# Performance work log

Hardware: AMD Instinct MI355X
Metric: run time of the kernel (lower is better)

## Reference

```python
import jax, jax.numpy as jnp
import numpy as np


def setup_inputs() -> dict:
    key = jax.random.key(0)
    ks = jax.random.split(key, 16)
    B, T, E, H, V = 64, 24, 512, 1024, 32000
    A = H  # attention_dim == hidden_size in original init
    s = 0.02  # init scale
    n = lambda k, shape: (jax.random.normal(k, shape, jnp.float32) * s)
    return {
        "features": jax.random.normal(ks[0], (B, E), jnp.float32),
        "captions": jax.random.randint(ks[1], (B, T), 0, V, dtype=jnp.int32),
        "lengths": jnp.full((B, 1), T + 1, dtype=jnp.int32),
        # learned parameters
        "emb": n(ks[2], (V, E)),
        "We": n(ks[3], (E, A)), "be": jnp.zeros((A,), jnp.float32),
        "Wd": n(ks[4], (H, A)), "bd": jnp.zeros((A,), jnp.float32),
        "va": n(ks[5], (A,)), "ba": jnp.zeros((), jnp.float32),
        "Wih": n(ks[6], (E, H)), "bih": jnp.zeros((H,), jnp.float32),
        "Wic": n(ks[7], (E, H)), "bic": jnp.zeros((H,), jnp.float32),
        "Wfb": n(ks[8], (H, E)), "bfb": jnp.zeros((E,), jnp.float32),
        "Wi": n(ks[9], (2 * E, 4 * H)), "Wh": n(ks[10], (H, 4 * H)),
        "bl": jnp.zeros((4 * H,), jnp.float32),
        "Wo": n(ks[11], (H, V)), "bo": jnp.zeros((V,), jnp.float32),
    }


def reference(features, captions, lengths, emb, We, be, Wd, bd, va, ba,
              Wih, bih, Wic, bic, Wfb, bfb, Wi, Wh, bl, Wo, bo):
    T = captions.shape[1]
    # embeddings = [features ; embed(captions)] -> [B, T+1, E]
    embeds = jnp.concatenate([features[:, None, :], emb[captions]], axis=1)
    mean_e = embeds.mean(axis=1)
    h = mean_e @ Wih + bih  # init_h
    c = mean_e @ Wic + bic  # init_c
    att1 = embeds @ We + be  # encoder projection, precomputed [B, L, A]

    def step(carry, emb_t):
        h, c = carry
        # additive attention over the full encoded sequence
        score = jnp.einsum('bla,a->bl', jax.nn.relu(att1 + (h @ Wd + bd)[:, None, :]), va) + ba
        alpha = jax.nn.softmax(score, axis=1)
        awe = jnp.einsum('bl,ble->be', alpha, embeds)
        gate = jax.nn.sigmoid(h @ Wfb + bfb)
        x = jnp.concatenate([emb_t, gate * awe], axis=-1)  # [B, 2E]
        z = x @ Wi + h @ Wh + bl
        i, f, g, o = jnp.split(z, 4, axis=-1)  # torch LSTM gate order i,f,g,o
        c = jax.nn.sigmoid(f) * c + jax.nn.sigmoid(i) * jnp.tanh(g)
        h = jax.nn.sigmoid(o) * jnp.tanh(c)
        return (h, c), h @ Wo + bo

    emb_seq = jnp.swapaxes(embeds[:, :T, :], 0, 1)  # [T, B, E]
    (_, _), logits = jax.lax.scan(step, (h, c), emb_seq)
    return jnp.swapaxes(logits, 0, 1)  # [B, T, V]
```

## Files before the change

### kernel.cpp

```cpp
#include <hip/hip_runtime.h>
#include <cstdio>
#include <cstdint>

#define B_ 64
#define T_ 24
#define L_ 25
#define E_ 512
#define H_ 1024
#define A_ 1024
#define V_ 32000
#define HCAT 5632

typedef unsigned short u16;
typedef short bf16x8 __attribute__((ext_vector_type(8)));
typedef float f32x4 __attribute__((ext_vector_type(4)));

__device__ __forceinline__ u16 f2bf(float f) {
    union { float f; unsigned int u; } v; v.f = f;
    unsigned int u = v.u;
    unsigned int r = (u + 0x7FFFu + ((u >> 16) & 1u)) >> 16;
    return (u16)r;
}
__device__ __forceinline__ float bf2f(u16 h) {
    union { unsigned int u; float f; } v; v.u = ((unsigned int)h) << 16;
    return v.f;
}
__device__ __forceinline__ void splitbf(float a, u16& hi, u16& lo) {
    hi = f2bf(a);
    lo = f2bf(a - bf2f(hi));
}
__device__ __forceinline__ float sigf(float x) { return 1.f / (1.f + __expf(-x)); }


__global__ void build_embeds(const float* __restrict__ features, const int* __restrict__ captions,
                             const float* __restrict__ emb, float* __restrict__ embeds,
                             float* __restrict__ mean_eT, u16* __restrict__ embsL2,
                             u16* __restrict__ embsA2) {
    int b = blockIdx.x; int e = threadIdx.x;
    float s = 0.f;
    for (int l = 0; l < L_; ++l) {
        float w;
        if (l == 0) w = features[b * E_ + e];
        else {
            int cap = captions[b * T_ + (l - 1)];
            w = emb[(size_t)cap * E_ + e];
        }
        embeds[(size_t)(b * L_ + l) * E_ + e] = w;
        s += w;
        u16 hi, lo; splitbf(w, hi, lo);
        size_t rl = (size_t)(b * L_ + l) * 1536;
        embsL2[rl + e] = hi; embsL2[rl + 512 + e] = lo; embsL2[rl + 1024 + e] = hi;
        if (l < T_) {
            size_t ra = (size_t)(l * 64 + b) * 1536;
            embsA2[ra + e] = hi; embsA2[ra + 512 + e] = lo; embsA2[ra + 1024 + e] = hi;
        }
    }
    mean_eT[e * B_ + b] = s * (1.f / 25.f);
}

__global__ void transpose_wo(const float* __restrict__ Wo, u16* __restrict__ WoT) {
    __shared__ float tile[32][33];
    int n0 = blockIdx.x * 32, k0 = blockIdx.y * 32;
    int tid = threadIdx.x;
    int tx = tid & 31, ty = tid >> 5;
    for (int i = ty; i < 32; i += 8)
        tile[i][tx] = Wo[(size_t)(k0 + i) * V_ + n0 + tx];
    __syncthreads();
    for (int i = ty; i < 32; i += 8)
        WoT[(size_t)(n0 + i) * H_ + k0 + tx] = f2bf(tile[tx][i]);
}

__global__ void tsplit(const float* __restrict__ W, u16* __restrict__ dst, int K, int srcld) {
    __shared__ float tile[32][33];
    int n0 = blockIdx.x * 32, k0 = blockIdx.y * 32;
    int tid = threadIdx.x;
    int tx = tid & 31, ty = tid >> 5;
    for (int i = ty; i < 32; i += 8)
        tile[i][tx] = W[(size_t)(k0 + i) * srcld + n0 + tx];
    __syncthreads();
    for (int i = ty; i < 32; i += 8) {
        float v = tile[tx][i];
        u16 hi, lo; splitbf(v, hi, lo);
        u16* d = dst + (size_t)(n0 + i) * (3 * K) + (k0 + tx);
        d[0] = hi; d[K] = hi; d[2 * K] = lo;
    }
}

__global__ __launch_bounds__(1024) void init_hc(const float* __restrict__ mean_eT,
                                                const float* __restrict__ Wih, const float* __restrict__ bih,
                                                const float* __restrict__ Wic, const float* __restrict__ bic,
                                                u16* __restrict__ h2, float* __restrict__ c) {
    int tid = threadIdx.x; int ny = tid & 15, r = tid >> 4;
    int col = blockIdx.x * 16 + ny;
    int cc = (col < H_) ? col : col - H_;
    const float* Wp = (col < H_) ? Wih : Wic;
    const float* bp = (col < H_) ? bih : bic;
    float acc = bp[cc];
    for (int k = 0; k < E_; ++k) acc += mean_eT[k * B_ + r] * Wp[(size_t)k * H_ + cc];
    if (col < H_) {
        u16 hi, lo; splitbf(acc, hi, lo);
        h2[(size_t)r * 3072 + cc] = hi;
        h2[(size_t)r * 3072 + 1024 + cc] = lo;
        h2[(size_t)r * 3072 + 2048 + cc] = hi;
    } else c[r * H_ + cc] = acc;
}

template<int BM, int BN>
__global__ __launch_bounds__(256) void gemm_split(const u16* __restrict__ A2, const u16* __restrict__ B2T,
                                                  const float* __restrict__ bias, float* __restrict__ C,
                                                  int K3, int ldc) {
    constexpr int LDS = 40;
    __shared__ u16 As[BM * LDS];
    __shared__ u16 Bs[BN * LDS];
    constexpr int FM = BM / 32, FN = BN / 32;
    constexpr int ACH = BM / 64, BCH = BN / 64;
    int m0 = blockIdx.x * BM, n0 = blockIdx.y * BN;
    int tid = threadIdx.x, lane = tid & 63, wid = tid >> 6;
    int wm = wid >> 1, wn = wid & 1;

    f32x4 acc[FM][FN];
#pragma unroll
    for (int m = 0; m < FM; ++m)
#pragma unroll
        for (int n = 0; n < FN; ++n) acc[m][n] = (f32x4){0.f, 0.f, 0.f, 0.f};

    const u16* agp[ACH]; u16* asw[ACH];
    const u16* bgp[BCH]; u16* bsw[BCH];
#pragma unroll
    for (int i = 0; i < ACH; ++i) {
        int id = i * 256 + tid; int row = id >> 2, q = id & 3;
        agp[i] = A2 + (size_t)(m0 + row) * K3 + q * 8;
        asw[i] = As + row * LDS + q * 8;
    }
#pragma unroll
    for (int i = 0; i < BCH; ++i) {
        int id = i * 256 + tid; int row = id >> 2, q = id & 3;
        bgp[i] = B2T + (size_t)(n0 + row) * K3 + q * 8;
        bsw[i] = Bs + row * LDS + q * 8;
    }
    int rsel = lane & 15, kg = (lane >> 4) * 8;
    const u16* ard[FM]; const u16* brd[FN];
#pragma unroll
    for (int m = 0; m < FM; ++m) ard[m] = As + (wm * (BM / 2) + m * 16 + rsel) * LDS + kg;
#pragma unroll
    for (int n = 0; n < FN; ++n) brd[n] = Bs + (wn * (BN / 2) + n * 16 + rsel) * LDS + kg;

    uint4 ar[ACH], br[BCH];
#pragma unroll
    for (int i = 0; i < ACH; ++i) ar[i] = *(const uint4*)(agp[i]);
#pragma unroll
    for (int i = 0; i < BCH; ++i) br[i] = *(const uint4*)(bgp[i]);

    int nk = K3 / 32;
    for (int k = 0; k < nk; ++k) {
#pragma unroll
        for (int i = 0; i < ACH; ++i) *(uint4*)(asw[i]) = ar[i];
#pragma unroll
        for (int i = 0; i < BCH; ++i) *(uint4*)(bsw[i]) = br[i];
        __syncthreads();
        if (k + 1 < nk) {
            int kt = (k + 1) * 32;
#pragma unroll
            for (int i = 0; i < ACH; ++i) ar[i] = *(const uint4*)(agp[i] + kt);
#pragma unroll
            for (int i = 0; i < BCH; ++i) br[i] = *(const uint4*)(bgp[i] + kt);
        }
        bf16x8 aF[FM], bF[FN];
#pragma unroll
        for (int m = 0; m < FM; ++m) aF[m] = *(const bf16x8*)(ard[m]);
#pragma unroll
        for (int n = 0; n < FN; ++n) bF[n] = *(const bf16x8*)(brd[n]);
#pragma unroll
        for (int m = 0; m < FM; ++m)
#pragma unroll
            for (int n = 0; n < FN; ++n)
                acc[m][n] = __builtin_amdgcn_mfma_f32_16x16x32_bf16(aF[m], bF[n], acc[m][n], 0, 0, 0);
        __syncthreads();
    }

    int r4 = (lane >> 4) * 4, cn = lane & 15;
#pragma unroll
    for (int n = 0; n < FN; ++n) {
        int gcol = n0 + wn * (BN / 2) + n * 16 + cn;
        float bv = bias[gcol];
#pragma unroll
        for (int m = 0; m < FM; ++m) {
            int gr = m0 + wm * (BM / 2) + m * 16 + r4;
#pragma unroll
            for (int reg = 0; reg < 4; ++reg)
                C[(size_t)(gr + reg) * ldc + gcol] = acc[m][n][reg] + bv;
        }
    }
}

template<int KITERS>
__global__ __launch_bounds__(256, 2) void gemm_sk(const u16* __restrict__ A2, const u16* __restrict__ B2T,
                                                  float* __restrict__ part, int K3, int N) {
    constexpr int BK = 128;
    constexpr int LDS = BK + 8;
    __shared__ u16 As[64 * LDS];
    __shared__ u16 Bs[64 * LDS];
    int n0 = blockIdx.x * 64;
    int ky = blockIdx.y;
    int k0 = ky * (BK * KITERS);
    int tid = threadIdx.x, lane = tid & 63, wid = tid >> 6;
    int wm = wid >> 1, wn = wid & 1;

    f32x4 acc[2][2];
#pragma unroll
    for (int m = 0; m < 2; ++m)
#pragma unroll
        for (int n = 0; n < 2; ++n) acc[m][n] = (f32x4){0.f, 0.f, 0.f, 0.f};

    int srow = tid >> 4, scq = tid & 15;
    const u16* agp[4]; u16* asw[4];
    const u16* bgp[4]; u16* bsw[4];
#pragma unroll
    for (int i = 0; i < 4; ++i) {
        int row = srow + i * 16;
        agp[i] = A2 + (size_t)row * K3 + k0 + scq * 8;
        asw[i] = As + row * LDS + scq * 8;
        bgp[i] = B2T + (size_t)(n0 + row) * K3 + k0 + scq * 8;
        bsw[i] = Bs + row * LDS + scq * 8;
    }
    int rsel = lane & 15, kg = (lane >> 4) * 8;
    const u16* ard[2]; const u16* brd[2];
#pragma unroll
    for (int m = 0; m < 2; ++m) ard[m] = As + (wm * 32 + m * 16 + rsel) * LDS + kg;
#pragma unroll
    for (int n = 0; n < 2; ++n) brd[n] = Bs + (wn * 32 + n * 16 + rsel) * LDS + kg;

    uint4 ar[4], br[4];
#pragma unroll
    for (int i = 0; i < 4; ++i) { ar[i] = *(const uint4*)(agp[i]); br[i] = *(const uint4*)(bgp[i]); }

    for (int it = 0; it < KITERS; ++it) {
#pragma unroll
        for (int i = 0; i < 4; ++i) { *(uint4*)(asw[i]) = ar[i]; *(uint4*)(bsw[i]) = br[i]; }
        __syncthreads();
        if (it + 1 < KITERS) {
            int kt = (it + 1) * BK;
#pragma unroll
            for (int i = 0; i < 4; ++i) {
                ar[i] = *(const uint4*)(agp[i] + kt);
                br[i] = *(const uint4*)(bgp[i] + kt);
            }
        }
#pragma unroll
        for (int kk = 0; kk < BK / 32; ++kk) {
            bf16x8 aF[2], bF[2];
#pragma unroll
            for (int m = 0; m < 2; ++m) aF[m] = *(const bf16x8*)(ard[m] + kk * 32);
#pragma unroll
            for (int n = 0; n < 2; ++n) bF[n] = *(const bf16x8*)(brd[n] + kk * 32);
#pragma unroll
            for (int m = 0; m < 2; ++m)
#pragma unroll
                for (int n = 0; n < 2; ++n)
                    acc[m][n] = __builtin_amdgcn_mfma_f32_16x16x32_bf16(aF[m], bF[n], acc[m][n], 0, 0, 0);
        }
        __syncthreads();
    }

    float* p = part + (size_t)ky * 64 * N;
    int r4 = (lane >> 4) * 4, cn = lane & 15;
#pragma unroll
    for (int n = 0; n < 2; ++n) {
        int gcol = n0 + wn * 32 + n * 16 + cn;
#pragma unroll
        for (int m = 0; m < 2; ++m) {
            int gr = wm * 32 + m * 16 + r4;
#pragma unroll
            for (int reg = 0; reg < 4; ++reg)
                p[(size_t)(gr + reg) * N + gcol] = acc[m][n][reg];
        }
    }
}


__global__ __launch_bounds__(256) void step_attn(const float* __restrict__ hpart, const float* __restrict__ att1,
                                                 const float* __restrict__ embeds, const float* __restrict__ va,
                                                 const float* __restrict__ bd, const float* __restrict__ bfb,
                                                 u16* __restrict__ x2s) {
    __shared__ float proj_s[1024], va_s[1024], sc_s[32], al_s[32];
    int b = blockIdx.x; int tid = threadIdx.x; int lane = tid & 63; int w = tid >> 6;
    for (int i = tid; i < 1024; i += 256) {
        float s = bd[i];
#pragma unroll
        for (int ky = 0; ky < 6; ++ky) s += hpart[(size_t)ky * 64 * HCAT + b * HCAT + i];
        proj_s[i] = s; va_s[i] = va[i];
    }
    __syncthreads();
    for (int l = w; l < L_; l += 4) {
        const float* arow = att1 + (size_t)(b * L_ + l) * A_;
        float p = 0.f;
        for (int a = lane; a < A_; a += 64) {
            float v = arow[a] + proj_s[a];
            p += fmaxf(v, 0.f) * va_s[a];
        }
        for (int off = 32; off; off >>= 1) p += __shfl_down(p, off);
        if (lane == 0) sc_s[l] = p;
    }
    __syncthreads();
    if (w == 0) {
        float s = (lane < L_) ? sc_s[lane] : -1e30f;
        float m = s;
        for (int off = 32; off; off >>= 1) m = fmaxf(m, __shfl_xor(m, off));
        float e = (lane < L_) ? __expf(s - m) : 0.f;
        float sum = e;
        for (int off = 32; off; off >>= 1) sum += __shfl_xor(sum, off);
        if (lane < L_) al_s[lane] = e / sum;
    }
    __syncthreads();
    for (int e = tid; e < E_; e += 256) {
        float aw = 0.f;
        for (int l = 0; l < L_; ++l) aw += al_s[l] * embeds[(size_t)(b * L_ + l) * E_ + e];
        float gp = bfb[e];
#pragma unroll
        for (int ky = 0; ky < 6; ++ky) gp += hpart[(size_t)ky * 64 * HCAT + b * HCAT + 1024 + e];
        float v = sigf(gp) * aw;
        u16 hi, lo; splitbf(v, hi, lo);
        x2s[(size_t)b * 1536 + e] = hi;
        x2s[(size_t)b * 1536 + 512 + e] = lo;
        x2s[(size_t)b * 1536 + 1024 + e] = hi;
    }
}

__global__ __launch_bounds__(256) void step_lstm(const float* __restrict__ zpart, const float* __restrict__ P1,
                                                 const float* __restrict__ hpart, float* __restrict__ c,
                                                 u16* __restrict__ h2, u16* __restrict__ hs_bf, int t) {
    int idx = blockIdx.x * 256 + threadIdx.x;
    int b = idx >> 10, n = idx & 1023;
    float zv[4];
#pragma unroll
    for (int g = 0; g < 4; ++g) {
        int col = g * 1024 + n;
        float s = P1[(size_t)(t * 64 + b) * 4096 + col];
#pragma unroll
        for (int ky = 0; ky < 3; ++ky) s += zpart[(size_t)ky * 64 * 4096 + b * 4096 + col];
#pragma unroll
        for (int ky = 0; ky < 6; ++ky) s += hpart[(size_t)ky * 64 * HCAT + b * HCAT + 1536 + col];
        zv[g] = s;
    }
    float cold = c[b * H_ + n];
    float cnew = sigf(zv[1]) * cold + sigf(zv[0]) * tanhf(zv[2]);
    float hh = sigf(zv[3]) * tanhf(cnew);
    c[b * H_ + n] = cnew;
    u16 hi, lo; splitbf(hh, hi, lo);
    h2[(size_t)b * 3072 + n] = hi;
    h2[(size_t)b * 3072 + 1024 + n] = lo;
    h2[(size_t)b * 3072 + 2048 + n] = hi;
    hs_bf[(size_t)(t * 64 + b) * 1024 + n] = f2bf(hh);
}

#define BMG 128
#define BNG 128
#define LDSS 40
#define NWG_M (T_ * B_ / BMG)
#define NWG_N (V_ / BNG)
#define NWG (NWG_M * NWG_N)

__global__ __launch_bounds__(256) void gemm_logits(const u16* __restrict__ Abf, const u16* __restrict__ Bbf,
                                                   const float* __restrict__ bo, float* __restrict__ out) {
    __shared__ u16 As[BMG * LDSS];
    __shared__ u16 Bs[BNG * LDSS];
    int lid = blockIdx.x;
    int wg = (lid & 7) * (NWG / 8) + (lid >> 3);
    int m0 = (wg % NWG_M) * BMG;
    int n0 = (wg / NWG_M) * BNG;
    int tid = threadIdx.x; int lane = tid & 63; int wid = tid >> 6;
    int wm = wid >> 1, wn = wid & 1;

    f32x4 acc[4][4];
#pragma unroll
    for (int m = 0; m < 4; ++m)
#pragma unroll
        for (int n = 0; n < 4; ++n) acc[m][n] = (f32x4){0.f, 0.f, 0.f, 0.f};

    int srow = tid >> 1;
    int shalf = tid & 1;
    const u16* ag = Abf + (size_t)(m0 + srow) * H_ + shalf * 16;
    const u16* bg = Bbf + (size_t)(n0 + srow) * H_ + shalf * 16;
    u16* asw = As + srow * LDSS + shalf * 16;
    u16* bsw = Bs + srow * LDSS + shalf * 16;

    int rsel = (lane & 15);
    int kg = (lane >> 4) * 8;

    uint4 a0 = *(const uint4*)(ag), a1 = *(const uint4*)(ag + 8);
    uint4 b0 = *(const uint4*)(bg), b1 = *(const uint4*)(bg + 8);

    for (int kt = 0; kt < H_; kt += 32) {
        *(uint4*)(asw) = a0; *(uint4*)(asw + 8) = a1;
        *(uint4*)(bsw) = b0; *(uint4*)(bsw + 8) = b1;
        __syncthreads();
        if (kt + 32 < H_) {
            a0 = *(const uint4*)(ag + kt + 32); a1 = *(const uint4*)(ag + kt + 40);
            b0 = *(const uint4*)(bg + kt + 32); b1 = *(const uint4*)(bg + kt + 40);
        }
        bf16x8 aF[4], bF[4];
#pragma unroll
        for (int m = 0; m < 4; ++m)
            aF[m] = *(const bf16x8*)(As + (wm * 64 + m * 16 + rsel) * LDSS + kg);
#pragma unroll
        for (int n = 0; n < 4; ++n)
            bF[n] = *(const bf16x8*)(Bs + (wn * 64 + n * 16 + rsel) * LDSS + kg);
#pragma unroll
        for (int m = 0; m < 4; ++m)
#pragma unroll
            for (int n = 0; n < 4; ++n)
                acc[m][n] = __builtin_amdgcn_mfma_f32_16x16x32_bf16(aF[m], bF[n], acc[m][n], 0, 0, 0);
        __syncthreads();
    }

    int r4 = (lane >> 4) * 4;
    int cn = lane & 15;
#pragma unroll
    for (int n = 0; n < 4; ++n) {
        int gn = n0 + wn * 64 + n * 16 + cn;
        float bv = bo[gn];
#pragma unroll
        for (int m = 0; m < 4; ++m) {
            int gmb = m0 + wm * 64 + m * 16 + r4;
#pragma unroll
            for (int reg = 0; reg < 4; ++reg) {
                int gm = gmb + reg;
                int b = gm & 63, t = gm >> 6;
                out[(size_t)(b * T_ + t) * V_ + gn] = acc[m][n][reg] + bv;
            }
        }
    }
}

extern "C" void kernel_launch(void* const* d_in, const int* in_sizes, int n_in,
                              void* d_out, int out_size, void* d_ws, size_t ws_size,
                              hipStream_t stream) {
    const float* features = (const float*)d_in[0];
    const int*   captions = (const int*)d_in[1];
    const float* emb = (const float*)d_in[3];
    const float* We  = (const float*)d_in[4];
    const float* be  = (const float*)d_in[5];
    const float* Wd  = (const float*)d_in[6];
    const float* bd  = (const float*)d_in[7];
    const float* va  = (const float*)d_in[8];
    const float* Wih = (const float*)d_in[10];
    const float* bih = (const float*)d_in[11];
    const float* Wic = (const float*)d_in[12];
    const float* bic = (const float*)d_in[13];
    const float* Wfb = (const float*)d_in[14];
    const float* bfb = (const float*)d_in[15];
    const float* Wi  = (const float*)d_in[16];
    const float* Wh  = (const float*)d_in[17];
    const float* bl  = (const float*)d_in[18];
    const float* Wo  = (const float*)d_in[19];
    const float* bo  = (const float*)d_in[20];
    float* out = (float*)d_out;

    char* ws = (char*)d_ws; size_t wo = 0;
    auto walloc = [&](size_t bytes) -> void* {
        void* p = ws + wo; wo += (bytes + 255) & ~(size_t)255; return p;
    };
    float* embeds  = (float*)walloc((size_t)B_ * L_ * E_ * 4);
    float* mean_eT = (float*)walloc((size_t)E_ * B_ * 4);
    u16*   embsL2  = (u16*)walloc((size_t)B_ * L_ * 1536 * 2);
    u16*   embsA2  = (u16*)walloc((size_t)T_ * B_ * 1536 * 2);
    u16*   h2      = (u16*)walloc((size_t)B_ * 3072 * 2);
    float* c       = (float*)walloc((size_t)B_ * H_ * 4);
    u16*   x2s     = (u16*)walloc((size_t)B_ * 1536 * 2);
    u16*   hs_bf   = (u16*)walloc((size_t)T_ * B_ * H_ * 2);
    u16*   WoT     = (u16*)walloc((size_t)V_ * H_ * 2);
    float* hpart   = (float*)walloc((size_t)6 * B_ * HCAT * 4);
    float* zpart   = (float*)walloc((size_t)3 * B_ * 4096 * 4);
    if (wo > ws_size) {
        fprintf(stderr, "kernel_launch: ws too small: need %zu have %zu\n", wo, ws_size);
        return;
    }

    char* ob = (char*)d_out; size_t oo = 0;
    auto oalloc = [&](size_t bytes) -> void* {
        void* p = ob + oo; oo += (bytes + 255) & ~(size_t)255; return p;
    };
    float* P1     = (float*)oalloc((size_t)T_ * B_ * 4096 * 4);
    u16*   WcatT2 = (u16*)oalloc((size_t)HCAT * 3072 * 2);
    u16*   WiT2a  = (u16*)oalloc((size_t)4096 * 1536 * 2);
    u16*   WiT2b  = (u16*)oalloc((size_t)4096 * 1536 * 2);
    u16*   WeT2   = (u16*)oalloc((size_t)1024 * 1536 * 2);
    float* att1   = (float*)oalloc((size_t)B_ * L_ * A_ * 4);

    build_embeds<<<B_, E_, 0, stream>>>(features, captions, emb, embeds, mean_eT, embsL2, embsA2);
    transpose_wo<<<dim3(V_ / 32, H_ / 32), 256, 0, stream>>>(Wo, WoT);
    tsplit<<<dim3(1024 / 32, 1024 / 32), 256, 0, stream>>>(Wd, WcatT2, 1024, 1024);
    tsplit<<<dim3(512 / 32, 1024 / 32), 256, 0, stream>>>(Wfb, WcatT2 + (size_t)1024 * 3072, 1024, 512);
    tsplit<<<dim3(4096 / 32, 1024 / 32), 256, 0, stream>>>(Wh, WcatT2 + (size_t)1536 * 3072, 1024, 4096);
    tsplit<<<dim3(4096 / 32, 512 / 32), 256, 0, stream>>>(Wi, WiT2a, 512, 4096);
    tsplit<<<dim3(4096 / 32, 512 / 32), 256, 0, stream>>>(Wi + (size_t)512 * 4096, WiT2b, 512, 4096);
    tsplit<<<dim3(1024 / 32, 512 / 32), 256, 0, stream>>>(We, WeT2, 512, 1024);
    init_hc<<<2 * H_ / 16, 1024, 0, stream>>>(mean_eT, Wih, bih, Wic, bic, h2, c);
    gemm_split<64, 64><<<dim3(1600 / 64, 1024 / 64), 256, 0, stream>>>(embsL2, WeT2, be, att1, 1536, 1024);
    gemm_split<128, 64><<<dim3(1536 / 128, 4096 / 64), 256, 0, stream>>>(embsA2, WiT2a, bl, P1, 1536, 4096);

    for (int t = 0; t < T_; ++t) {
        gemm_sk<4><<<dim3(HCAT / 64, 6), 256, 0, stream>>>(h2, WcatT2, hpart, 3072, HCAT);
        step_attn<<<B_, 256, 0, stream>>>(hpart, att1, embeds, va, bd, bfb, x2s);
        gemm_sk<4><<<dim3(4096 / 64, 3), 256, 0, stream>>>(x2s, WiT2b, zpart, 1536, 4096);
        step_lstm<<<B_ * H_ / 256, 256, 0, stream>>>(zpart, P1, hpart, c, h2, hs_bf, t);
    }

    gemm_logits<<<NWG, 256, 0, stream>>>(hs_bf, WoT, bo, out);
}
```

Before: 2.576 ms.

## Fuse recurrent loop into persistent kernel with grid barriers, merge weight prep kernels

```diff
diff --git a/kernel.cpp b/kernel.cpp
--- a/kernel.cpp
+++ b/kernel.cpp
@@ -58,23 +58,33 @@
     mean_eT[e * B_ + b] = s * (1.f / 25.f);
 }
 
-__global__ void transpose_wo(const float* __restrict__ Wo, u16* __restrict__ WoT) {
+__global__ __launch_bounds__(256) void prep_weights(
+    const float* __restrict__ Wo, const float* __restrict__ Wd, const float* __restrict__ Wfb,
+    const float* __restrict__ Wh, const float* __restrict__ Wi, const float* __restrict__ We,
+    u16* __restrict__ WoT, u16* __restrict__ WcatT2, u16* __restrict__ WiT2a,
+    u16* __restrict__ WiT2b, u16* __restrict__ WeT2) {
     __shared__ float tile[32][33];
-    int n0 = blockIdx.x * 32, k0 = blockIdx.y * 32;
-    int tid = threadIdx.x;
-    int tx = tid & 31, ty = tid >> 5;
-    for (int i = ty; i < 32; i += 8)
-        tile[i][tx] = Wo[(size_t)(k0 + i) * V_ + n0 + tx];
-    __syncthreads();
-    for (int i = ty; i < 32; i += 8)
-        WoT[(size_t)(n0 + i) * H_ + k0 + tx] = f2bf(tile[tx][i]);
-}
-
-__global__ void tsplit(const float* __restrict__ W, u16* __restrict__ dst, int K, int srcld) {
-    __shared__ float tile[32][33];
-    int n0 = blockIdx.x * 32, k0 = blockIdx.y * 32;
-    int tid = threadIdx.x;
-    int tx = tid & 31, ty = tid >> 5;
+    int id = blockIdx.x;
+    int tid = threadIdx.x, tx = tid & 31, ty = tid >> 5;
+    if (id < 32000) {
+        int nx = id % 1000, ky = id / 1000;
+        int n0 = nx * 32, k0 = ky * 32;
+        for (int i = ty; i < 32; i += 8)
+            tile[i][tx] = Wo[(size_t)(k0 + i) * V_ + n0 + tx];
+        __syncthreads();
+        for (int i = ty; i < 32; i += 8)
+            WoT[(size_t)(n0 + i) * H_ + k0 + tx] = f2bf(tile[tx][i]);
+        return;
+    }
+    id -= 32000;
+    const float* W; u16* dst; int K, srcld, tilesx;
+    if (id < 1024)      {             W = Wd;  dst = WcatT2;                        K = 1024; srcld = 1024; tilesx = 32; }
+    else if (id < 1536) { id -= 1024; W = Wfb; dst = WcatT2 + (size_t)1024 * 3072;  K = 1024; srcld = 512;  tilesx = 16; }
+    else if (id < 5632) { id -= 1536; W = Wh;  dst = WcatT2 + (size_t)1536 * 3072;  K = 1024; srcld = 4096; tilesx = 128; }
+    else if (id < 7680) { id -= 5632; W = Wi;  dst = WiT2a;                         K = 512;  srcld = 4096; tilesx = 128; }
+    else if (id < 9728) { id -= 7680; W = Wi + (size_t)512 * 4096; dst = WiT2b;     K = 512;  srcld = 4096; tilesx = 128; }
+    else                { id -= 9728; W = We;  dst = WeT2;                          K = 512;  srcld = 1024; tilesx = 32; }
+    int n0 = (id % tilesx) * 32, k0 = (id / tilesx) * 32;
     for (int i = ty; i < 32; i += 8)
         tile[i][tx] = W[(size_t)(k0 + i) * srcld + n0 + tx];
     __syncthreads();
@@ -109,7 +119,7 @@
 __global__ __launch_bounds__(256) void gemm_split(const u16* __restrict__ A2, const u16* __restrict__ B2T,
                                                   const float* __restrict__ bias, float* __restrict__ C,
                                                   int K3, int ldc) {
-    constexpr int LDS = 40;
+    constexpr int LDS = 34;
     __shared__ u16 As[BM * LDS];
     __shared__ u16 Bs[BN * LDS];
     constexpr int FM = BM / 32, FN = BN / 32;
@@ -193,169 +203,232 @@
     }
 }
 
-template<int KITERS>
-__global__ __launch_bounds__(256, 2) void gemm_sk(const u16* __restrict__ A2, const u16* __restrict__ B2T,
-                                                  float* __restrict__ part, int K3, int N) {
-    constexpr int BK = 128;
-    constexpr int LDS = BK + 8;
-    __shared__ u16 As[64 * LDS];
-    __shared__ u16 Bs[64 * LDS];
-    int n0 = blockIdx.x * 64;
-    int ky = blockIdx.y;
-    int k0 = ky * (BK * KITERS);
-    int tid = threadIdx.x, lane = tid & 63, wid = tid >> 6;
+#define LDA_ 138
+#define NBLK 256
+
+__device__ __forceinline__ void gridbar(unsigned* cnt, unsigned* gen, unsigned ep) {
+    __syncthreads();
+    if (threadIdx.x == 0)
+        __hip_atomic_fetch_add(&cnt[blockIdx.x & 63], 1u, __ATOMIC_ACQ_REL, __HIP_MEMORY_SCOPE_AGENT);
+    if (blockIdx.x == 0) {
+        if (threadIdx.x < 64) {
+            while (__hip_atomic_load(&cnt[threadIdx.x], __ATOMIC_ACQUIRE, __HIP_MEMORY_SCOPE_AGENT) < 4u * ep)
+                __builtin_amdgcn_s_sleep(1);
+        }
+        __syncthreads();
+        if (threadIdx.x == 0)
+            __hip_atomic_store(gen, ep, __ATOMIC_RELEASE, __HIP_MEMORY_SCOPE_AGENT);
+    } else {
+        if (threadIdx.x == 0) {
+            while (__hip_atomic_load(gen, __ATOMIC_ACQUIRE, __HIP_MEMORY_SCOPE_AGENT) < ep)
+                __builtin_amdgcn_s_sleep(1);
+        }
+    }
+    __syncthreads();
+}
+
+__device__ __forceinline__ void mm64_tile(
+    const u16* ag0, const u16* ag1, const u16* ag2, const u16* ag3,
+    const u16* bg0, const u16* bg1, const u16* bg2, const u16* bg3,
+    u16* asw, u16* bsw,
+    const u16* ard0, const u16* ard1, const u16* brd0, const u16* brd1,
+    int iters, f32x4 (&acc)[2][2]) {
+    uint4 ar0 = *(const uint4*)ag0, ar1 = *(const uint4*)ag1, ar2 = *(const uint4*)ag2, ar3 = *(const uint4*)ag3;
+    uint4 br0 = *(const uint4*)bg0, br1 = *(const uint4*)bg1, br2 = *(const uint4*)bg2, br3 = *(const uint4*)bg3;
+    for (int it = 0; it < iters; ++it) {
+        *(uint4*)(asw) = ar0; *(uint4*)(asw + 16 * LDA_) = ar1;
+        *(uint4*)(asw + 32 * LDA_) = ar2; *(uint4*)(asw + 48 * LDA_) = ar3;
+        *(uint4*)(bsw) = br0; *(uint4*)(bsw + 16 * LDA_) = br1;
+        *(uint4*)(bsw + 32 * LDA_) = br2; *(uint4*)(bsw + 48 * LDA_) = br3;
+        __syncthreads();
+        if (it + 1 < iters) {
+            int kt = (it + 1) * 128;
+            ar0 = *(const uint4*)(ag0 + kt); ar1 = *(const uint4*)(ag1 + kt);
+            ar2 = *(const uint4*)(ag2 + kt); ar3 = *(const uint4*)(ag3 + kt);
+            br0 = *(const uint4*)(bg0 + kt); br1 = *(const uint4*)(bg1 + kt);
+            br2 = *(const uint4*)(bg2 + kt); br3 = *(const uint4*)(bg3 + kt);
+        }
+#pragma unroll
+        for (int kk = 0; kk < 4; ++kk) {
+            bf16x8 a0 = *(const bf16x8*)(ard0 + kk * 32);
+            bf16x8 a1 = *(const bf16x8*)(ard1 + kk * 32);
+            bf16x8 b0 = *(const bf16x8*)(brd0 + kk * 32);
+            bf16x8 b1 = *(const bf16x8*)(brd1 + kk * 32);
+            acc[0][0] = __builtin_amdgcn_mfma_f32_16x16x32_bf16(a0, b0, acc[0][0], 0, 0, 0);
+            acc[0][1] = __builtin_amdgcn_mfma_f32_16x16x32_bf16(a0, b1, acc[0][1], 0, 0, 0);
+            acc[1][0] = __builtin_amdgcn_mfma_f32_16x16x32_bf16(a1, b0, acc[1][0], 0, 0, 0);
+            acc[1][1] = __builtin_amdgcn_mfma_f32_16x16x32_bf16(a1, b1, acc[1][1], 0, 0, 0);
+        }
+        __syncthreads();
+    }
+}
+
+__global__ __launch_bounds__(256) void loop_fused(
+    u16* __restrict__ h2, float* __restrict__ c,
+    const u16* __restrict__ WcatT2, const float* __restrict__ bd, const float* __restrict__ bfb,
+    const float* __restrict__ att1, const float* __restrict__ embeds, const float* __restrict__ va,
+    u16* __restrict__ x2s, const u16* __restrict__ WiT2b, const float* __restrict__ P1,
+    float* __restrict__ hpart, u16* __restrict__ hs_bf,
+    unsigned* __restrict__ bar_cnt, unsigned* __restrict__ bar_gen) {
+    __shared__ u16 smem[2 * 64 * LDA_];
+    u16* As = smem;
+    u16* Bs = smem + 64 * LDA_;
+    int bid = blockIdx.x, tid = threadIdx.x;
+    int lane = tid & 63, wid = tid >> 6;
     int wm = wid >> 1, wn = wid & 1;
-
-    f32x4 acc[2][2];
-#pragma unroll
-    for (int m = 0; m < 2; ++m)
-#pragma unroll
-        for (int n = 0; n < 2; ++n) acc[m][n] = (f32x4){0.f, 0.f, 0.f, 0.f};
-
+    int rsel = lane & 15, kg = (lane >> 4) * 8;
+    int r4 = (lane >> 4) * 4, cn = lane & 15;
     int srow = tid >> 4, scq = tid & 15;
-    const u16* agp[4]; u16* asw[4];
-    const u16* bgp[4]; u16* bsw[4];
+
+    u16* asw = As + srow * LDA_ + scq * 8;
+    u16* bsw = Bs + srow * LDA_ + scq * 8;
+    const u16* ard0 = As + (wm * 32 + rsel) * LDA_ + kg;
+    const u16* ard1 = ard0 + 16 * LDA_;
+    const u16* brd0 = Bs + (wn * 32 + rsel) * LDA_ + kg;
+    const u16* brd1 = brd0 + 16 * LDA_;
+
+    int a_id = bid < 176 ? bid : 0;
+    int a_nt = a_id % 88, a_ky = a_id / 88;
+    const u16* a_ag[4]; const u16* a_bg[4];
 #pragma unroll
     for (int i = 0; i < 4; ++i) {
         int row = srow + i * 16;
-        agp[i] = A2 + (size_t)row * K3 + k0 + scq * 8;
-        asw[i] = As + row * LDS + scq * 8;
-        bgp[i] = B2T + (size_t)(n0 + row) * K3 + k0 + scq * 8;
-        bsw[i] = Bs + row * LDS + scq * 8;
-    }
-    int rsel = lane & 15, kg = (lane >> 4) * 8;
-    const u16* ard[2]; const u16* brd[2];
-#pragma unroll
-    for (int m = 0; m < 2; ++m) ard[m] = As + (wm * 32 + m * 16 + rsel) * LDS + kg;
-#pragma unroll
-    for (int n = 0; n < 2; ++n) brd[n] = Bs + (wn * 32 + n * 16 + rsel) * LDS + kg;
-
-    uint4 ar[4], br[4];
-#pragma unroll
-    for (int i = 0; i < 4; ++i) { ar[i] = *(const uint4*)(agp[i]); br[i] = *(const uint4*)(bgp[i]); }
-
-    for (int it = 0; it < KITERS; ++it) {
-#pragma unroll
-        for (int i = 0; i < 4; ++i) { *(uint4*)(asw[i]) = ar[i]; *(uint4*)(bsw[i]) = br[i]; }
-        __syncthreads();
-        if (it + 1 < KITERS) {
-            int kt = (it + 1) * BK;
-#pragma unroll
-            for (int i = 0; i < 4; ++i) {
-                ar[i] = *(const uint4*)(agp[i] + kt);
-                br[i] = *(const uint4*)(bgp[i] + kt);
-            }
-        }
-#pragma unroll
-        for (int kk = 0; kk < BK / 32; ++kk) {
-            bf16x8 aF[2], bF[2];
-#pragma unroll
-            for (int m = 0; m < 2; ++m) aF[m] = *(const bf16x8*)(ard[m] + kk * 32);
-#pragma unroll
-            for (int n = 0; n < 2; ++n) bF[n] = *(const bf16x8*)(brd[n] + kk * 32);
+        a_ag[i] = h2 + (size_t)row * 3072 + a_ky * 1536 + scq * 8;
+        a_bg[i] = WcatT2 + (size_t)(a_nt * 64 + row) * 3072 + a_ky * 1536 + scq * 8;
+    }
+    int z_n0 = (bid & 63) * 16;
+    const u16* z_ag[4]; const u16* z_bg[4];
+#pragma unroll
+    for (int i = 0; i < 4; ++i) {
+        int row = srow + i * 16;
+        z_ag[i] = x2s + (size_t)row * 1536 + scq * 8;
+        z_bg[i] = WiT2b + (size_t)((row >> 4) * 1024 + z_n0 + (row & 15)) * 1536 + scq * 8;
+    }
+
+    unsigned ep = 0;
+    for (int t = 0; t < T_; ++t) {
+        if (bid < 176) {
+            f32x4 acc[2][2];
 #pragma unroll
             for (int m = 0; m < 2; ++m)
 #pragma unroll
-                for (int n = 0; n < 2; ++n)
-                    acc[m][n] = __builtin_amdgcn_mfma_f32_16x16x32_bf16(aF[m], bF[n], acc[m][n], 0, 0, 0);
-        }
-        __syncthreads();
-    }
-
-    float* p = part + (size_t)ky * 64 * N;
-    int r4 = (lane >> 4) * 4, cn = lane & 15;
-#pragma unroll
-    for (int n = 0; n < 2; ++n) {
-        int gcol = n0 + wn * 32 + n * 16 + cn;
-#pragma unroll
-        for (int m = 0; m < 2; ++m) {
-            int gr = wm * 32 + m * 16 + r4;
-#pragma unroll
-            for (int reg = 0; reg < 4; ++reg)
-                p[(size_t)(gr + reg) * N + gcol] = acc[m][n][reg];
-        }
-    }
-}
-
-
-__global__ __launch_bounds__(256) void step_attn(const float* __restrict__ hpart, const float* __restrict__ att1,
-                                                 const float* __restrict__ embeds, const float* __restrict__ va,
-                                                 const float* __restrict__ bd, const float* __restrict__ bfb,
-                                                 u16* __restrict__ x2s) {
-    __shared__ float proj_s[1024], va_s[1024], sc_s[32], al_s[32];
-    int b = blockIdx.x; int tid = threadIdx.x; int lane = tid & 63; int w = tid >> 6;
-    for (int i = tid; i < 1024; i += 256) {
-        float s = bd[i];
-#pragma unroll
-        for (int ky = 0; ky < 6; ++ky) s += hpart[(size_t)ky * 64 * HCAT + b * HCAT + i];
-        proj_s[i] = s; va_s[i] = va[i];
-    }
-    __syncthreads();
-    for (int l = w; l < L_; l += 4) {
-        const float* arow = att1 + (size_t)(b * L_ + l) * A_;
-        float p = 0.f;
-        for (int a = lane; a < A_; a += 64) {
-            float v = arow[a] + proj_s[a];
-            p += fmaxf(v, 0.f) * va_s[a];
-        }
-        for (int off = 32; off; off >>= 1) p += __shfl_down(p, off);
-        if (lane == 0) sc_s[l] = p;
-    }
-    __syncthreads();
-    if (w == 0) {
-        float s = (lane < L_) ? sc_s[lane] : -1e30f;
-        float m = s;
-        for (int off = 32; off; off >>= 1) m = fmaxf(m, __shfl_xor(m, off));
-        float e = (lane < L_) ? __expf(s - m) : 0.f;
-        float sum = e;
-        for (int off = 32; off; off >>= 1) sum += __shfl_xor(sum, off);
-        if (lane < L_) al_s[lane] = e / sum;
-    }
-    __syncthreads();
-    for (int e = tid; e < E_; e += 256) {
-        float aw = 0.f;
-        for (int l = 0; l < L_; ++l) aw += al_s[l] * embeds[(size_t)(b * L_ + l) * E_ + e];
-        float gp = bfb[e];
-#pragma unroll
-        for (int ky = 0; ky < 6; ++ky) gp += hpart[(size_t)ky * 64 * HCAT + b * HCAT + 1024 + e];
-        float v = sigf(gp) * aw;
-        u16 hi, lo; splitbf(v, hi, lo);
-        x2s[(size_t)b * 1536 + e] = hi;
-        x2s[(size_t)b * 1536 + 512 + e] = lo;
-        x2s[(size_t)b * 1536 + 1024 + e] = hi;
-    }
-}
-
-__global__ __launch_bounds__(256) void step_lstm(const float* __restrict__ zpart, const float* __restrict__ P1,
-                                                 const float* __restrict__ hpart, float* __restrict__ c,
-                                                 u16* __restrict__ h2, u16* __restrict__ hs_bf, int t) {
-    int idx = blockIdx.x * 256 + threadIdx.x;
-    int b = idx >> 10, n = idx & 1023;
-    float zv[4];
-#pragma unroll
-    for (int g = 0; g < 4; ++g) {
-        int col = g * 1024 + n;
-        float s = P1[(size_t)(t * 64 + b) * 4096 + col];
-#pragma unroll
-        for (int ky = 0; ky < 3; ++ky) s += zpart[(size_t)ky * 64 * 4096 + b * 4096 + col];
-#pragma unroll
-        for (int ky = 0; ky < 6; ++ky) s += hpart[(size_t)ky * 64 * HCAT + b * HCAT + 1536 + col];
-        zv[g] = s;
-    }
-    float cold = c[b * H_ + n];
-    float cnew = sigf(zv[1]) * cold + sigf(zv[0]) * tanhf(zv[2]);
-    float hh = sigf(zv[3]) * tanhf(cnew);
-    c[b * H_ + n] = cnew;
-    u16 hi, lo; splitbf(hh, hi, lo);
-    h2[(size_t)b * 3072 + n] = hi;
-    h2[(size_t)b * 3072 + 1024 + n] = lo;
-    h2[(size_t)b * 3072 + 2048 + n] = hi;
-    hs_bf[(size_t)(t * 64 + b) * 1024 + n] = f2bf(hh);
+                for (int n = 0; n < 2; ++n) acc[m][n] = (f32x4){0.f, 0.f, 0.f, 0.f};
+            mm64_tile(a_ag[0], a_ag[1], a_ag[2], a_ag[3], a_bg[0], a_bg[1], a_bg[2], a_bg[3],
+                      asw, bsw, ard0, ard1, brd0, brd1, 12, acc);
+            float* p = hpart + (size_t)a_ky * 64 * HCAT;
+#pragma unroll
+            for (int n = 0; n < 2; ++n) {
+                int gcol = a_nt * 64 + wn * 32 + n * 16 + cn;
+#pragma unroll
+                for (int m = 0; m < 2; ++m) {
+                    int gr = wm * 32 + m * 16 + r4;
+#pragma unroll
+                    for (int reg = 0; reg < 4; ++reg)
+                        p[(size_t)(gr + reg) * HCAT + gcol] = acc[m][n][reg];
+                }
+            }
+        }
+        gridbar(bar_cnt, bar_gen, ++ep);
+
+        if (bid < 64) {
+            int b = bid;
+            float* proj_s = (float*)smem;
+            float* va_s = proj_s + 1024;
+            float* sc_s = va_s + 1024;
+            float* al_s = sc_s + 32;
+            for (int i = tid; i < 1024; i += 256) {
+                proj_s[i] = bd[i] + hpart[(size_t)b * HCAT + i] + hpart[(size_t)(64 + b) * HCAT + i];
+                va_s[i] = va[i];
+            }
+            __syncthreads();
+            for (int l = wid; l < L_; l += 4) {
+                const float* arow = att1 + (size_t)(b * L_ + l) * A_;
+                float p = 0.f;
+                for (int a = lane; a < A_; a += 64)
+                    p += fmaxf(arow[a] + proj_s[a], 0.f) * va_s[a];
+                for (int off = 32; off; off >>= 1) p += __shfl_down(p, off);
+                if (lane == 0) sc_s[l] = p;
+            }
+            __syncthreads();
+            if (wid == 0) {
+                float s = (lane < L_) ? sc_s[lane] : -1e30f;
+                float m = s;
+                for (int off = 32; off; off >>= 1) m = fmaxf(m, __shfl_xor(m, off));
+                float e = (lane < L_) ? __expf(s - m) : 0.f;
+                float sum = e;
+                for (int off = 32; off; off >>= 1) sum += __shfl_xor(sum, off);
+                if (lane < L_) al_s[lane] = e / sum;
+            }
+            __syncthreads();
+            for (int e = tid; e < E_; e += 256) {
+                float aw = 0.f;
+                for (int l = 0; l < L_; ++l) aw += al_s[l] * embeds[(size_t)(b * L_ + l) * E_ + e];
+                float gp = bfb[e] + hpart[(size_t)b * HCAT + 1024 + e] + hpart[(size_t)(64 + b) * HCAT + 1024 + e];
+                float v = sigf(gp) * aw;
+                u16 hi, lo; splitbf(v, hi, lo);
+                x2s[(size_t)b * 1536 + e] = hi;
+                x2s[(size_t)b * 1536 + 512 + e] = lo;
+                x2s[(size_t)b * 1536 + 1024 + e] = hi;
+            }
+        }
+        gridbar(bar_cnt, bar_gen, ++ep);
+
+        if (bid < 64) {
+            f32x4 acc[2][2];
+#pragma unroll
+            for (int m = 0; m < 2; ++m)
+#pragma unroll
+                for (int n = 0; n < 2; ++n) acc[m][n] = (f32x4){0.f, 0.f, 0.f, 0.f};
+            mm64_tile(z_ag[0], z_ag[1], z_ag[2], z_ag[3], z_bg[0], z_bg[1], z_bg[2], z_bg[3],
+                      asw, bsw, ard0, ard1, brd0, brd1, 12, acc);
+            float* zb = (float*)smem;
+#pragma unroll
+            for (int n = 0; n < 2; ++n) {
+                int gc = wn * 32 + n * 16 + cn;
+                int gate = gc >> 4, cc = gc & 15;
+                int col = gate * 1024 + z_n0 + cc;
+#pragma unroll
+                for (int m = 0; m < 2; ++m) {
+                    int grb = wm * 32 + m * 16 + r4;
+#pragma unroll
+                    for (int reg = 0; reg < 4; ++reg) {
+                        int gr = grb + reg;
+                        float zv = acc[m][n][reg]
+                                 + P1[(size_t)(t * 64 + gr) * 4096 + col]
+                                 + hpart[(size_t)gr * HCAT + 1536 + col]
+                                 + hpart[(size_t)(64 + gr) * HCAT + 1536 + col];
+                        zb[gc * 64 + gr] = zv;
+                    }
+                }
+            }
+            __syncthreads();
+#pragma unroll
+            for (int j = 0; j < 4; ++j) {
+                int cell = tid * 4 + j;
+                int b = cell >> 4, cc = cell & 15;
+                int nn = z_n0 + cc;
+                float zi = zb[(0 * 16 + cc) * 64 + b];
+                float zf = zb[(1 * 16 + cc) * 64 + b];
+                float zg = zb[(2 * 16 + cc) * 64 + b];
+                float zo = zb[(3 * 16 + cc) * 64 + b];
+                float cold = c[b * H_ + nn];
+                float cnew = sigf(zf) * cold + sigf(zi) * tanhf(zg);
+                float hh = sigf(zo) * tanhf(cnew);
+                c[b * H_ + nn] = cnew;
+                u16 hi, lo; splitbf(hh, hi, lo);
+                h2[(size_t)b * 3072 + nn] = hi;
+                h2[(size_t)b * 3072 + 1024 + nn] = lo;
+                h2[(size_t)b * 3072 + 2048 + nn] = hi;
+                hs_bf[(size_t)(t * 64 + b) * 1024 + nn] = f2bf(hh);
+            }
+        }
+        gridbar(bar_cnt, bar_gen, ++ep);
+    }
 }
 
 #define BMG 128
 #define BNG 128
-#define LDSS 40
+#define LDSS 34
 #define NWG_M (T_ * B_ / BMG)
 #define NWG_N (V_ / BNG)
 #define NWG (NWG_M * NWG_N)
@@ -469,8 +542,8 @@
     u16*   x2s     = (u16*)walloc((size_t)B_ * 1536 * 2);
     u16*   hs_bf   = (u16*)walloc((size_t)T_ * B_ * H_ * 2);
     u16*   WoT     = (u16*)walloc((size_t)V_ * H_ * 2);
-    float* hpart   = (float*)walloc((size_t)6 * B_ * HCAT * 4);
-    float* zpart   = (float*)walloc((size_t)3 * B_ * 4096 * 4);
+    float* hpart   = (float*)walloc((size_t)2 * B_ * HCAT * 4);
+    unsigned* bar  = (unsigned*)walloc(512);
     if (wo > ws_size) {
         fprintf(stderr, "kernel_launch: ws too small: need %zu have %zu\n", wo, ws_size);
         return;
@@ -487,24 +560,16 @@
     u16*   WeT2   = (u16*)oalloc((size_t)1024 * 1536 * 2);
     float* att1   = (float*)oalloc((size_t)B_ * L_ * A_ * 4);
 
+    hipMemsetAsync(bar, 0, 512, stream);
     build_embeds<<<B_, E_, 0, stream>>>(features, captions, emb, embeds, mean_eT, embsL2, embsA2);
-    transpose_wo<<<dim3(V_ / 32, H_ / 32), 256, 0, stream>>>(Wo, WoT);
-    tsplit<<<dim3(1024 / 32, 1024 / 32), 256, 0, stream>>>(Wd, WcatT2, 1024, 1024);
-    tsplit<<<dim3(512 / 32, 1024 / 32), 256, 0, stream>>>(Wfb, WcatT2 + (size_t)1024 * 3072, 1024, 512);
-    tsplit<<<dim3(4096 / 32, 1024 / 32), 256, 0, stream>>>(Wh, WcatT2 + (size_t)1536 * 3072, 1024, 4096);
-    tsplit<<<dim3(4096 / 32, 512 / 32), 256, 0, stream>>>(Wi, WiT2a, 512, 4096);
-    tsplit<<<dim3(4096 / 32, 512 / 32), 256, 0, stream>>>(Wi + (size_t)512 * 4096, WiT2b, 512, 4096);
-    tsplit<<<dim3(1024 / 32, 512 / 32), 256, 0, stream>>>(We, WeT2, 512, 1024);
+    prep_weights<<<32000 + 10240, 256, 0, stream>>>(Wo, Wd, Wfb, Wh, Wi, We,
+                                                    WoT, WcatT2, WiT2a, WiT2b, WeT2);
     init_hc<<<2 * H_ / 16, 1024, 0, stream>>>(mean_eT, Wih, bih, Wic, bic, h2, c);
     gemm_split<64, 64><<<dim3(1600 / 64, 1024 / 64), 256, 0, stream>>>(embsL2, WeT2, be, att1, 1536, 1024);
     gemm_split<128, 64><<<dim3(1536 / 128, 4096 / 64), 256, 0, stream>>>(embsA2, WiT2a, bl, P1, 1536, 4096);
 
-    for (int t = 0; t < T_; ++t) {
-        gemm_sk<4><<<dim3(HCAT / 64, 6), 256, 0, stream>>>(h2, WcatT2, hpart, 3072, HCAT);
-        step_attn<<<B_, 256, 0, stream>>>(hpart, att1, embeds, va, bd, bfb, x2s);
-        gemm_sk<4><<<dim3(4096 / 64, 3), 256, 0, stream>>>(x2s, WiT2b, zpart, 1536, 4096);
-        step_lstm<<<B_ * H_ / 256, 256, 0, stream>>>(zpart, P1, hpart, c, h2, hs_bf, t);
-    }
+    loop_fused<<<NBLK, 256, 0, stream>>>(h2, c, WcatT2, bd, bfb, att1, embeds, va,
+                                         x2s, WiT2b, P1, hpart, hs_bf, bar, bar + 64);
 
     gemm_logits<<<NWG, 256, 0, stream>>>(hs_bf, WoT, bo, out);
 }
```

New measurement: 8.290 ms. 222% more time.

## Fuse per-step input GEMM with LSTM cell and merge weight-prep launches

Applied to the files above, without the earlier changes.

```diff
diff --git a/kernel.cpp b/kernel.cpp
--- a/kernel.cpp
+++ b/kernel.cpp
@@ -58,23 +58,33 @@
     mean_eT[e * B_ + b] = s * (1.f / 25.f);
 }
 
-__global__ void transpose_wo(const float* __restrict__ Wo, u16* __restrict__ WoT) {
+__global__ __launch_bounds__(256) void prep_weights(
+    const float* __restrict__ Wo, const float* __restrict__ Wd, const float* __restrict__ Wfb,
+    const float* __restrict__ Wh, const float* __restrict__ Wi, const float* __restrict__ We,
+    u16* __restrict__ WoT, u16* __restrict__ WcatT2, u16* __restrict__ WiT2a,
+    u16* __restrict__ WiT2b, u16* __restrict__ WeT2) {
     __shared__ float tile[32][33];
-    int n0 = blockIdx.x * 32, k0 = blockIdx.y * 32;
-    int tid = threadIdx.x;
-    int tx = tid & 31, ty = tid >> 5;
-    for (int i = ty; i < 32; i += 8)
-        tile[i][tx] = Wo[(size_t)(k0 + i) * V_ + n0 + tx];
-    __syncthreads();
-    for (int i = ty; i < 32; i += 8)
-        WoT[(size_t)(n0 + i) * H_ + k0 + tx] = f2bf(tile[tx][i]);
-}
-
-__global__ void tsplit(const float* __restrict__ W, u16* __restrict__ dst, int K, int srcld) {
-    __shared__ float tile[32][33];
-    int n0 = blockIdx.x * 32, k0 = blockIdx.y * 32;
-    int tid = threadIdx.x;
-    int tx = tid & 31, ty = tid >> 5;
+    int id = blockIdx.x;
+    int tid = threadIdx.x, tx = tid & 31, ty = tid >> 5;
+    if (id < 32000) {
+        int nx = id % 1000, ky = id / 1000;
+        int n0 = nx * 32, k0 = ky * 32;
+        for (int i = ty; i < 32; i += 8)
+            tile[i][tx] = Wo[(size_t)(k0 + i) * V_ + n0 + tx];
+        __syncthreads();
+        for (int i = ty; i < 32; i += 8)
+            WoT[(size_t)(n0 + i) * H_ + k0 + tx] = f2bf(tile[tx][i]);
+        return;
+    }
+    id -= 32000;
+    const float* W; u16* dst; int K, srcld, tilesx;
+    if (id < 1024)      {             W = Wd;  dst = WcatT2;                        K = 1024; srcld = 1024; tilesx = 32; }
+    else if (id < 1536) { id -= 1024; W = Wfb; dst = WcatT2 + (size_t)1024 * 3072;  K = 1024; srcld = 512;  tilesx = 16; }
+    else if (id < 5632) { id -= 1536; W = Wh;  dst = WcatT2 + (size_t)1536 * 3072;  K = 1024; srcld = 4096; tilesx = 128; }
+    else if (id < 7680) { id -= 5632; W = Wi;  dst = WiT2a;                         K = 512;  srcld = 4096; tilesx = 128; }
+    else if (id < 9728) { id -= 7680; W = Wi + (size_t)512 * 4096; dst = WiT2b;     K = 512;  srcld = 4096; tilesx = 128; }
+    else                { id -= 9728; W = We;  dst = WeT2;                          K = 512;  srcld = 1024; tilesx = 32; }
+    int n0 = (id % tilesx) * 32, k0 = (id / tilesx) * 32;
     for (int i = ty; i < 32; i += 8)
         tile[i][tx] = W[(size_t)(k0 + i) * srcld + n0 + tx];
     __syncthreads();
@@ -109,7 +119,7 @@
 __global__ __launch_bounds__(256) void gemm_split(const u16* __restrict__ A2, const u16* __restrict__ B2T,
                                                   const float* __restrict__ bias, float* __restrict__ C,
                                                   int K3, int ldc) {
-    constexpr int LDS = 40;
+    constexpr int LDS = 34;
     __shared__ u16 As[BM * LDS];
     __shared__ u16 Bs[BN * LDS];
     constexpr int FM = BM / 32, FN = BN / 32;
@@ -326,36 +336,116 @@
     }
 }
 
-__global__ __launch_bounds__(256) void step_lstm(const float* __restrict__ zpart, const float* __restrict__ P1,
-                                                 const float* __restrict__ hpart, float* __restrict__ c,
-                                                 u16* __restrict__ h2, u16* __restrict__ hs_bf, int t) {
-    int idx = blockIdx.x * 256 + threadIdx.x;
-    int b = idx >> 10, n = idx & 1023;
-    float zv[4];
-#pragma unroll
-    for (int g = 0; g < 4; ++g) {
-        int col = g * 1024 + n;
-        float s = P1[(size_t)(t * 64 + b) * 4096 + col];
-#pragma unroll
-        for (int ky = 0; ky < 3; ++ky) s += zpart[(size_t)ky * 64 * 4096 + b * 4096 + col];
-#pragma unroll
-        for (int ky = 0; ky < 6; ++ky) s += hpart[(size_t)ky * 64 * HCAT + b * HCAT + 1536 + col];
-        zv[g] = s;
-    }
-    float cold = c[b * H_ + n];
-    float cnew = sigf(zv[1]) * cold + sigf(zv[0]) * tanhf(zv[2]);
-    float hh = sigf(zv[3]) * tanhf(cnew);
-    c[b * H_ + n] = cnew;
-    u16 hi, lo; splitbf(hh, hi, lo);
-    h2[(size_t)b * 3072 + n] = hi;
-    h2[(size_t)b * 3072 + 1024 + n] = lo;
-    h2[(size_t)b * 3072 + 2048 + n] = hi;
-    hs_bf[(size_t)(t * 64 + b) * 1024 + n] = f2bf(hh);
+#define LDA_ 138
+__global__ __launch_bounds__(256) void step_zlstm(const u16* __restrict__ x2s, const u16* __restrict__ WiT2b,
+                                                  const float* __restrict__ P1, const float* __restrict__ hpart,
+                                                  float* __restrict__ c, u16* __restrict__ h2,
+                                                  u16* __restrict__ hs_bf, int t) {
+    __shared__ u16 smem[2 * 64 * LDA_];
+    u16* As = smem;
+    u16* Bs = smem + 64 * LDA_;
+    int tid = threadIdx.x, lane = tid & 63, wid = tid >> 6;
+    int wm = wid >> 1, wn = wid & 1;
+    int rsel = lane & 15, kg = (lane >> 4) * 8;
+    int r4 = (lane >> 4) * 4, cn = lane & 15;
+    int srow = tid >> 4, scq = tid & 15;
+    int z_n0 = blockIdx.x * 16;
+
+    u16* asw = As + srow * LDA_ + scq * 8;
+    u16* bsw = Bs + srow * LDA_ + scq * 8;
+    const u16* ard0 = As + (wm * 32 + rsel) * LDA_ + kg;
+    const u16* ard1 = ard0 + 16 * LDA_;
+    const u16* brd0 = Bs + (wn * 32 + rsel) * LDA_ + kg;
+    const u16* brd1 = brd0 + 16 * LDA_;
+
+    const u16* zA[4]; const u16* zB[4];
+#pragma unroll
+    for (int i = 0; i < 4; ++i) {
+        int row = srow + i * 16;
+        zA[i] = x2s + (size_t)row * 1536 + scq * 8;
+        zB[i] = WiT2b + (size_t)((row >> 4) * 1024 + z_n0 + (row & 15)) * 1536 + scq * 8;
+    }
+
+    f32x4 acc[2][2];
+#pragma unroll
+    for (int m = 0; m < 2; ++m)
+#pragma unroll
+        for (int n = 0; n < 2; ++n) acc[m][n] = (f32x4){0.f, 0.f, 0.f, 0.f};
+
+    uint4 ar0 = *(const uint4*)zA[0], ar1 = *(const uint4*)zA[1], ar2 = *(const uint4*)zA[2], ar3 = *(const uint4*)zA[3];
+    uint4 br0 = *(const uint4*)zB[0], br1 = *(const uint4*)zB[1], br2 = *(const uint4*)zB[2], br3 = *(const uint4*)zB[3];
+    for (int it = 0; it < 12; ++it) {
+        *(uint4*)(asw) = ar0; *(uint4*)(asw + 16 * LDA_) = ar1;
+        *(uint4*)(asw + 32 * LDA_) = ar2; *(uint4*)(asw + 48 * LDA_) = ar3;
+        *(uint4*)(bsw) = br0; *(uint4*)(bsw + 16 * LDA_) = br1;
+        *(uint4*)(bsw + 32 * LDA_) = br2; *(uint4*)(bsw + 48 * LDA_) = br3;
+        __syncthreads();
+        if (it + 1 < 12) {
+            int kt = (it + 1) * 128;
+            ar0 = *(const uint4*)(zA[0] + kt); ar1 = *(const uint4*)(zA[1] + kt);
+            ar2 = *(const uint4*)(zA[2] + kt); ar3 = *(const uint4*)(zA[3] + kt);
+            br0 = *(const uint4*)(zB[0] + kt); br1 = *(const uint4*)(zB[1] + kt);
+            br2 = *(const uint4*)(zB[2] + kt); br3 = *(const uint4*)(zB[3] + kt);
+        }
+#pragma unroll
+        for (int kk = 0; kk < 4; ++kk) {
+            bf16x8 a0 = *(const bf16x8*)(ard0 + kk * 32);
+            bf16x8 a1 = *(const bf16x8*)(ard1 + kk * 32);
+            bf16x8 b0 = *(const bf16x8*)(brd0 + kk * 32);
+            bf16x8 b1 = *(const bf16x8*)(brd1 + kk * 32);
+            acc[0][0] = __builtin_amdgcn_mfma_f32_16x16x32_bf16(a0, b0, acc[0][0], 0, 0, 0);
+            acc[0][1] = __builtin_amdgcn_mfma_f32_16x16x32_bf16(a0, b1, acc[0][1], 0, 0, 0);
+            acc[1][0] = __builtin_amdgcn_mfma_f32_16x16x32_bf16(a1, b0, acc[1][0], 0, 0, 0);
+            acc[1][1] = __builtin_amdgcn_mfma_f32_16x16x32_bf16(a1, b1, acc[1][1], 0, 0, 0);
+        }
+        __syncthreads();
+    }
+
+    float* zb = (float*)smem;
+#pragma unroll
+    for (int n = 0; n < 2; ++n) {
+        int gc = wn * 32 + n * 16 + cn;
+        int gate = gc >> 4, cc = gc & 15;
+        int col = gate * 1024 + z_n0 + cc;
+#pragma unroll
+        for (int m = 0; m < 2; ++m) {
+            int grb = wm * 32 + m * 16 + r4;
+#pragma unroll
+            for (int reg = 0; reg < 4; ++reg) {
+                int gr = grb + reg;
+                float zv = acc[m][n][reg] + P1[(size_t)(t * 64 + gr) * 4096 + col];
+#pragma unroll
+                for (int ky = 0; ky < 6; ++ky)
+                    zv += hpart[(size_t)ky * 64 * HCAT + gr * HCAT + 1536 + col];
+                zb[gc * 64 + gr] = zv;
+            }
+        }
+    }
+    __syncthreads();
+#pragma unroll
+    for (int j = 0; j < 4; ++j) {
+        int cell = tid * 4 + j;
+        int b = cell >> 4, cc = cell & 15;
+        int nn = z_n0 + cc;
+        float zi = zb[(0 * 16 + cc) * 64 + b];
+        float zf = zb[(1 * 16 + cc) * 64 + b];
+        float zg = zb[(2 * 16 + cc) * 64 + b];
+        float zo = zb[(3 * 16 + cc) * 64 + b];
+        float cold = c[b * H_ + nn];
+        float cnew = sigf(zf) * cold + sigf(zi) * tanhf(zg);
+        float hh = sigf(zo) * tanhf(cnew);
+        c[b * H_ + nn] = cnew;
+        u16 hi, lo; splitbf(hh, hi, lo);
+        h2[(size_t)b * 3072 + nn] = hi;
+        h2[(size_t)b * 3072 + 1024 + nn] = lo;
+        h2[(size_t)b * 3072 + 2048 + nn] = hi;
+        hs_bf[(size_t)(t * 64 + b) * 1024 + nn] = f2bf(hh);
+    }
 }
 
 #define BMG 128
 #define BNG 128
-#define LDSS 40
+#define LDSS 34
 #define NWG_M (T_ * B_ / BMG)
 #define NWG_N (V_ / BNG)
 #define NWG (NWG_M * NWG_N)
@@ -470,7 +560,6 @@
     u16*   hs_bf   = (u16*)walloc((size_t)T_ * B_ * H_ * 2);
     u16*   WoT     = (u16*)walloc((size_t)V_ * H_ * 2);
     float* hpart   = (float*)walloc((size_t)6 * B_ * HCAT * 4);
-    float* zpart   = (float*)walloc((size_t)3 * B_ * 4096 * 4);
     if (wo > ws_size) {
         fprintf(stderr, "kernel_launch: ws too small: need %zu have %zu\n", wo, ws_size);
         return;
@@ -488,13 +577,8 @@
     float* att1   = (float*)oalloc((size_t)B_ * L_ * A_ * 4);
 
     build_embeds<<<B_, E_, 0, stream>>>(features, captions, emb, embeds, mean_eT, embsL2, embsA2);
-    transpose_wo<<<dim3(V_ / 32, H_ / 32), 256, 0, stream>>>(Wo, WoT);
-    tsplit<<<dim3(1024 / 32, 1024 / 32), 256, 0, stream>>>(Wd, WcatT2, 1024, 1024);
-    tsplit<<<dim3(512 / 32, 1024 / 32), 256, 0, stream>>>(Wfb, WcatT2 + (size_t)1024 * 3072, 1024, 512);
-    tsplit<<<dim3(4096 / 32, 1024 / 32), 256, 0, stream>>>(Wh, WcatT2 + (size_t)1536 * 3072, 1024, 4096);
-    tsplit<<<dim3(4096 / 32, 512 / 32), 256, 0, stream>>>(Wi, WiT2a, 512, 4096);
-    tsplit<<<dim3(4096 / 32, 512 / 32), 256, 0, stream>>>(Wi + (size_t)512 * 4096, WiT2b, 512, 4096);
-    tsplit<<<dim3(1024 / 32, 512 / 32), 256, 0, stream>>>(We, WeT2, 512, 1024);
+    prep_weights<<<32000 + 10240, 256, 0, stream>>>(Wo, Wd, Wfb, Wh, Wi, We,
+                                                    WoT, WcatT2, WiT2a, WiT2b, WeT2);
     init_hc<<<2 * H_ / 16, 1024, 0, stream>>>(mean_eT, Wih, bih, Wic, bic, h2, c);
     gemm_split<64, 64><<<dim3(1600 / 64, 1024 / 64), 256, 0, stream>>>(embsL2, WeT2, be, att1, 1536, 1024);
     gemm_split<128, 64><<<dim3(1536 / 128, 4096 / 64), 256, 0, stream>>>(embsA2, WiT2a, bl, P1, 1536, 4096);
@@ -502,8 +586,7 @@
     for (int t = 0; t < T_; ++t) {
         gemm_sk<4><<<dim3(HCAT / 64, 6), 256, 0, stream>>>(h2, WcatT2, hpart, 3072, HCAT);
         step_attn<<<B_, 256, 0, stream>>>(hpart, att1, embeds, va, bd, bfb, x2s);
-        gemm_sk<4><<<dim3(4096 / 64, 3), 256, 0, stream>>>(x2s, WiT2b, zpart, 1536, 4096);
-        step_lstm<<<B_ * H_ / 256, 256, 0, stream>>>(zpart, P1, hpart, c, h2, hs_bf, t);
+        step_zlstm<<<H_ / 16, 256, 0, stream>>>(x2s, WiT2b, P1, hpart, c, h2, hs_bf, t);
     }
 
     gemm_logits<<<NWG, 256, 0, stream>>>(hs_bf, WoT, bo, out);
```

Result: slower. 3.308 ms (+28.4%).
